# Optimization experiments

Hardware: AMD Instinct MI355X
Metric: run time of the kernel (lower is better)

## Reference

```python
import jax, jax.numpy as jnp
import numpy as np

NUM_USERS = 100000
NUM_ITEMS = 50000
NUM_NODES = NUM_USERS + NUM_ITEMS
EMBED_DIM = 64
NUM_LAYERS = 3
NUM_EDGES = 1200000


def setup_inputs() -> dict:
    key = jax.random.key(0)
    k1, k2 = jax.random.split(key)
    edge_index = jax.random.randint(k1, (2, NUM_EDGES), 0, NUM_NODES, dtype=jnp.int32)
    # xavier_uniform for [N, D]
    limit = float(np.sqrt(6.0 / (NUM_NODES + EMBED_DIM)))
    embedding = jax.random.uniform(k2, (NUM_NODES, EMBED_DIM), dtype=jnp.float32,
                                   minval=-limit, maxval=limit)
    return {"edge_index": edge_index, "embedding": embedding}


def reference(edge_index, embedding):
    n = embedding.shape[0]
    row, col = edge_index[0], edge_index[1]
    ones = jnp.ones((edge_index.shape[1],), dtype=embedding.dtype)
    deg_row = jax.ops.segment_sum(ones, row, num_segments=n)
    deg_col = jax.ops.segment_sum(ones, col, num_segments=n)
    # deg^-0.5 with inf (deg==0) -> 0
    inv_row = jnp.where(deg_row > 0, jax.lax.rsqrt(jnp.maximum(deg_row, 1e-30)), 0.0)
    inv_col = jnp.where(deg_col > 0, jax.lax.rsqrt(jnp.maximum(deg_col, 1e-30)), 0.0)
    norm = (inv_row[row] * inv_col[col])[:, None]  # [E, 1]

    x = embedding
    accum = x
    for _ in range(NUM_LAYERS):
        # gather source embeddings, scale by symmetric norm, scatter-add at target
        msgs = norm * x[row]                       # [E, D]
        x = jax.ops.segment_sum(msgs, col, num_segments=n)
        accum = accum + x
    final = accum / jnp.asarray(NUM_LAYERS + 1, dtype=embedding.dtype)
    return final[:NUM_USERS], final[NUM_USERS:]
```

## Files before the change

kernel.cpp:

```cpp
#include <hip/hip_runtime.h>
#include <hip/hip_fp16.h>


constexpr int NUM_USERS = 100000;
constexpr int NUM_ITEMS = 50000;
constexpr int N_NODES   = NUM_USERS + NUM_ITEMS;
constexpr int EMBED_DIM = 64;
constexpr int NUM_EDGES = 1200000;
constexpr int SHIFT = 9;
constexpr int BSZ   = 1 << SHIFT;
constexpr int NBUCK = (N_NODES + BSZ - 1) >> SHIFT;
constexpr int EPB   = 8192;
constexpr int P1_BLOCKS = (NUM_EDGES + EPB - 1) / EPB;
constexpr int CAPB  = 64;
constexpr int FIXCAP  = 32;
constexpr int FIXHALF = 16;

__global__ void __launch_bounds__(1024)
pass1_bin(const int4* __restrict__ row4, const int4* __restrict__ col4,
          unsigned int* __restrict__ binned_c, unsigned short* __restrict__ binned_r,
          int* __restrict__ cnts_c, int* __restrict__ cnts_r) {
    __shared__ int cur_c[NBUCK], cur_r[NBUCK];
    int t = threadIdx.x, blk = blockIdx.x;
    for (int i = t; i < NBUCK; i += 1024) { cur_c[i] = 0; cur_r[i] = 0; }
    __syncthreads();
    constexpr int NV = NUM_EDGES / 4;
    int base4 = blk * 2048;
#pragma unroll
    for (int k = 0; k < 2; ++k) {
        int v = base4 + k * 1024 + t;
        if (v < NV) {
            int4 c = col4[v];
            int4 r = row4[v];
            int cc[4] = {c.x, c.y, c.z, c.w};
            int rr[4] = {r.x, r.y, r.z, r.w};
#pragma unroll
            for (int q = 0; q < 4; ++q) {
                int dc = cc[q] >> SHIFT;
                int sc = atomicAdd(&cur_c[dc], 1);
                if (sc < CAPB)
                    binned_c[(dc * P1_BLOCKS + blk) * CAPB + sc] =
                        ((unsigned)(cc[q] & (BSZ - 1)) << 18) | (unsigned)rr[q];
                int dr = rr[q] >> SHIFT;
                int sr = atomicAdd(&cur_r[dr], 1);
                if (sr < CAPB)
                    binned_r[(dr * P1_BLOCKS + blk) * CAPB + sr] =
                        (unsigned short)(rr[q] & (BSZ - 1));
            }
        }
    }
    __syncthreads();
    for (int i = t; i < NBUCK; i += 1024) {
        cnts_c[blk * NBUCK + i] = cur_c[i];
        cnts_r[blk * NBUCK + i] = cur_r[i];
    }
}

__global__ void __launch_bounds__(512)
pass2_place(const unsigned int* __restrict__ binned_c, const unsigned short* __restrict__ binned_r,
            const int* __restrict__ cnts_c, const int* __restrict__ cnts_r,
            int* __restrict__ fixed_idx, ushort2* __restrict__ deg2) {
    __shared__ int cur[BSZ];
    __shared__ int cnt_l[P1_BLOCKS];
    int t = threadIdx.x;
    cur[t] = 0;
    int b = blockIdx.x;
    constexpr int TOT = P1_BLOCKS * CAPB;
    if (b < NBUCK) {
        for (int i = t; i < P1_BLOCKS; i += 512) cnt_l[i] = cnts_c[i * NBUCK + b];
        __syncthreads();
        const unsigned int* src = binned_c + (size_t)b * TOT;
        for (int i = t; i < TOT; i += 512) {
            int cnt = cnt_l[i >> 6]; if (cnt > CAPB) cnt = CAPB;
            if ((i & 63) < cnt) {
                unsigned int w = src[i];
                int lc = (int)(w >> 18);
                int r  = (int)(w & 0x3FFFFu);
                int slot = atomicAdd(&cur[lc], 1);
                if (slot < FIXCAP)
                    fixed_idx[(((b << SHIFT) | lc) << 5) + slot] = r;
            }
        }
        __syncthreads();
        int node = (b << SHIFT) + t;
        if (node < N_NODES) deg2[node].x = (unsigned short)cur[t];
    } else {
        int bb = b - NBUCK;
        for (int i = t; i < P1_BLOCKS; i += 512) cnt_l[i] = cnts_r[i * NBUCK + bb];
        __syncthreads();
        const unsigned short* src = binned_r + (size_t)bb * TOT;
        for (int i = t; i < TOT; i += 512) {
            int cnt = cnt_l[i >> 6]; if (cnt > CAPB) cnt = CAPB;
            if ((i & 63) < cnt) atomicAdd(&cur[src[i]], 1);
        }
        __syncthreads();
        int node = (bb << SHIFT) + t;
        if (node < N_NODES) deg2[node].y = (unsigned short)cur[t];
    }
}

__global__ void init_y_kernel(const unsigned int* __restrict__ deg2w,
                              const float4* __restrict__ emb4, int2* __restrict__ y0) {
    int i = blockIdx.x * blockDim.x + threadIdx.x;
    if (i < N_NODES * (EMBED_DIM / 4)) {
        int dr = (int)(deg2w[i >> 4] >> 16);
        float w = (dr > 0) ? rsqrtf((float)dr) : 0.0f;
        float4 e = emb4[i];
        __half2 h0 = __floats2half2_rn(w * e.x, w * e.y);
        __half2 h1 = __floats2half2_rn(w * e.z, w * e.w);
        y0[i] = make_int2(*reinterpret_cast<int*>(&h0), *reinterpret_cast<int*>(&h1));
    }
}

__device__ __forceinline__ void acc8(float* f, const int4& v) {
    float2 a0 = __half22float2(*reinterpret_cast<const __half2*>(&v.x));
    float2 a1 = __half22float2(*reinterpret_cast<const __half2*>(&v.y));
    float2 a2 = __half22float2(*reinterpret_cast<const __half2*>(&v.z));
    float2 a3 = __half22float2(*reinterpret_cast<const __half2*>(&v.w));
    f[0] += a0.x; f[1] += a0.y; f[2] += a1.x; f[3] += a1.y;
    f[4] += a2.x; f[5] += a2.y; f[6] += a3.x; f[7] += a3.y;
}

__global__ void __launch_bounds__(256, 8)
layer_kernel(const unsigned int* __restrict__ deg2w,
             const int* __restrict__ fixed_idx,
             const int4* __restrict__ y_src,
             int4* __restrict__ y_dst,
             int4* __restrict__ x_acc,
             float4* __restrict__ out4,
             const float4* __restrict__ emb4,
             int mode) {
    int wv = (blockIdx.x * blockDim.x + threadIdx.x) >> 6;
    int nA = wv << 1;
    if (nA >= N_NODES) return;
    int nB = nA | 1;
    int lane = threadIdx.x & 63;
    int d4 = lane & 7;
    int e  = lane >> 3;
    int sl = lane & 15;

    int recA = fixed_idx[(nA << 5) | sl];
    int recB = fixed_idx[(nB << 5) | sl];
    uint2 dd = reinterpret_cast<const uint2*>(deg2w)[wv];
    int4 xv;
    float4 o0, o1;
    if (e == 2 || e == 3) {
        int n = (e == 2) ? nA : nB;
        if (mode != 0) xv = x_acc[n * 8 + d4];
        if (mode == 2) { o0 = emb4[n * 16 + d4 * 2]; o1 = emb4[n * 16 + d4 * 2 + 1]; }
    }

    int crA = (int)(dd.x & 0xFFFFu), drA = (int)(dd.x >> 16);
    int crB = (int)(dd.y & 0xFFFFu), drB = (int)(dd.y >> 16);
    int cntA = (crA < FIXCAP) ? crA : FIXCAP;
    int cntB = (crB < FIXCAP) ? crB : FIXCAP;
    float invcA = (crA > 0) ? rsqrtf((float)crA) : 0.0f;
    float invcB = (crB > 0) ? rsqrtf((float)crB) : 0.0f;
    float invrA = (drA > 0) ? rsqrtf((float)drA) : 0.0f;
    float invrB = (drB > 0) ? rsqrtf((float)drB) : 0.0f;
    int idxA = (sl < cntA) ? recA : 0;
    int idxB = (sl < cntB) ? recB : 0;

    float fA[8] = {0.f, 0.f, 0.f, 0.f, 0.f, 0.f, 0.f, 0.f};
    float fB[8] = {0.f, 0.f, 0.f, 0.f, 0.f, 0.f, 0.f, 0.f};

    if (cntA <= FIXHALF && cntB <= FIXHALF) {
        int s0A = __shfl(idxA, e);
        int s1A = __shfl(idxA, 8 + e);
        int s0B = __shfl(idxB, e);
        int s1B = __shfl(idxB, 8 + e);
        int4 vaA = y_src[s0A * 8 + d4];
        int4 vbA = y_src[s1A * 8 + d4];
        int4 vaB = y_src[s0B * 8 + d4];
        int4 vbB = y_src[s1B * 8 + d4];
        if (e < cntA)     acc8(fA, vaA);
        if (8 + e < cntA) acc8(fA, vbA);
        if (e < cntB)     acc8(fB, vaB);
        if (8 + e < cntB) acc8(fB, vbB);
    } else {
        {
            int rec2 = fixed_idx[(nA << 5) | 16 | sl];
            int idx2 = ((16 | sl) < cntA) ? rec2 : 0;
            int s0 = __shfl(idxA, e),     s1 = __shfl(idxA, 8 + e);
            int s2 = __shfl(idx2, e),     s3 = __shfl(idx2, 8 + e);
            int4 va = y_src[s0 * 8 + d4], vb = y_src[s1 * 8 + d4];
            int4 vc = y_src[s2 * 8 + d4], vd = y_src[s3 * 8 + d4];
            if (e < cntA)      acc8(fA, va);
            if (8 + e < cntA)  acc8(fA, vb);
            if (16 + e < cntA) acc8(fA, vc);
            if (24 + e < cntA) acc8(fA, vd);
        }
        {
            int rec2 = fixed_idx[(nB << 5) | 16 | sl];
            int idx2 = ((16 | sl) < cntB) ? rec2 : 0;
            int s0 = __shfl(idxB, e),     s1 = __shfl(idxB, 8 + e);
            int s2 = __shfl(idx2, e),     s3 = __shfl(idx2, 8 + e);
            int4 va = y_src[s0 * 8 + d4], vb = y_src[s1 * 8 + d4];
            int4 vc = y_src[s2 * 8 + d4], vd = y_src[s3 * 8 + d4];
            if (e < cntB)      acc8(fB, va);
            if (8 + e < cntB)  acc8(fB, vb);
            if (16 + e < cntB) acc8(fB, vc);
            if (24 + e < cntB) acc8(fB, vd);
        }
    }

#pragma unroll
    for (int k = 0; k < 8; ++k) {
        fA[k] += __shfl_xor(fA[k], 8);
        fA[k] += __shfl_xor(fA[k], 16);
        fA[k] += __shfl_xor(fA[k], 32);
        fB[k] += __shfl_xor(fB[k], 8);
        fB[k] += __shfl_xor(fB[k], 16);
        fB[k] += __shfl_xor(fB[k], 32);
    }
#pragma unroll
    for (int k = 0; k < 8; ++k) { fA[k] *= invcA; fB[k] *= invcB; }

    if (mode != 2) {
        if (e == 0 || e == 1) {
            int n = (e == 0) ? nA : nB;
            float invr = (e == 0) ? invrA : invrB;
            const float* f = (e == 0) ? fA : fB;
            __half2 p0 = __floats2half2_rn(invr * f[0], invr * f[1]);
            __half2 p1 = __floats2half2_rn(invr * f[2], invr * f[3]);
            __half2 p2 = __floats2half2_rn(invr * f[4], invr * f[5]);
            __half2 p3 = __floats2half2_rn(invr * f[6], invr * f[7]);
            int4 st;
            st.x = *reinterpret_cast<int*>(&p0);
            st.y = *reinterpret_cast<int*>(&p1);
            st.z = *reinterpret_cast<int*>(&p2);
            st.w = *reinterpret_cast<int*>(&p3);
            y_dst[n * 8 + d4] = st;
        } else if (e == 2 || e == 3) {
            int n = (e == 2) ? nA : nB;
            const float* f = (e == 2) ? fA : fB;
            float g[8];
            if (mode == 1) {
                float2 b0 = __half22float2(*reinterpret_cast<const __half2*>(&xv.x));
                float2 b1 = __half22float2(*reinterpret_cast<const __half2*>(&xv.y));
                float2 b2 = __half22float2(*reinterpret_cast<const __half2*>(&xv.z));
                float2 b3 = __half22float2(*reinterpret_cast<const __half2*>(&xv.w));
                g[0] = b0.x + f[0]; g[1] = b0.y + f[1]; g[2] = b1.x + f[2]; g[3] = b1.y + f[3];
                g[4] = b2.x + f[4]; g[5] = b2.y + f[5]; g[6] = b3.x + f[6]; g[7] = b3.y + f[7];
            } else {
#pragma unroll
                for (int k = 0; k < 8; ++k) g[k] = f[k];
            }
            __half2 q0 = __floats2half2_rn(g[0], g[1]);
            __half2 q1 = __floats2half2_rn(g[2], g[3]);
            __half2 q2 = __floats2half2_rn(g[4], g[5]);
            __half2 q3 = __floats2half2_rn(g[6], g[7]);
            int4 st;
            st.x = *reinterpret_cast<int*>(&q0);
            st.y = *reinterpret_cast<int*>(&q1);
            st.z = *reinterpret_cast<int*>(&q2);
            st.w = *reinterpret_cast<int*>(&q3);
            x_acc[n * 8 + d4] = st;
        }
    } else if (e == 2 || e == 3) {
        int n = (e == 2) ? nA : nB;
        const float* f = (e == 2) ? fA : fB;
        float2 b0 = __half22float2(*reinterpret_cast<const __half2*>(&xv.x));
        float2 b1 = __half22float2(*reinterpret_cast<const __half2*>(&xv.y));
        float2 b2 = __half22float2(*reinterpret_cast<const __half2*>(&xv.z));
        float2 b3 = __half22float2(*reinterpret_cast<const __half2*>(&xv.w));
        o0.x = (o0.x + b0.x + f[0]) * 0.25f; o0.y = (o0.y + b0.y + f[1]) * 0.25f;
        o0.z = (o0.z + b1.x + f[2]) * 0.25f; o0.w = (o0.w + b1.y + f[3]) * 0.25f;
        o1.x = (o1.x + b2.x + f[4]) * 0.25f; o1.y = (o1.y + b2.y + f[5]) * 0.25f;
        o1.z = (o1.z + b3.x + f[6]) * 0.25f; o1.w = (o1.w + b3.y + f[7]) * 0.25f;
        int ob = n * 16 + d4 * 2;
        out4[ob]     = o0;
        out4[ob + 1] = o1;
    }
}

extern "C" void kernel_launch(void* const* d_in, const int* in_sizes, int n_in,
                              void* d_out, int out_size, void* d_ws, size_t ws_size,
                              hipStream_t stream) {
    const int*   edge_index = (const int*)d_in[0];
    const float* embedding  = (const float*)d_in[1];
    const int* row = edge_index;
    const int* col = edge_index + NUM_EDGES;
    float* out = (float*)d_out;

    char* ws = (char*)d_ws;
    auto align_up = [](size_t v) { return (v + 255) & ~size_t(255); };
    size_t off = 0;
    ushort2* deg2    = (ushort2*)(ws + off); off = align_up(off + sizeof(ushort2) * N_NODES);
    int* cnts_c      = (int*)(ws + off); off = align_up(off + sizeof(int) * P1_BLOCKS * NBUCK);
    int* cnts_r      = (int*)(ws + off); off = align_up(off + sizeof(int) * P1_BLOCKS * NBUCK);
    int* fixed_idx   = (int*)(ws + off); off = align_up(off + sizeof(int) * N_NODES * FIXCAP);
    __half2* ya      = (__half2*)(ws + off); off = align_up(off + sizeof(__half2) * N_NODES * 32);
    __half2* yb      = (__half2*)(ws + off); off = align_up(off + sizeof(__half2) * N_NODES * 32);
    __half2* xa      = (__half2*)(ws + off); off = align_up(off + sizeof(__half2) * N_NODES * 32);
    unsigned int*   binned_c = (unsigned int*)d_out;
    unsigned short* binned_r = (unsigned short*)ya;

    pass1_bin<<<P1_BLOCKS, 1024, 0, stream>>>((const int4*)row, (const int4*)col,
                                              binned_c, binned_r, cnts_c, cnts_r);
    pass2_place<<<2 * NBUCK, 512, 0, stream>>>(binned_c, binned_r, cnts_c, cnts_r,
                                               fixed_idx, deg2);
    {
        int n4 = N_NODES * 16;
        int threads = 256, blocks = (n4 + threads - 1) / threads;
        init_y_kernel<<<blocks, threads, 0, stream>>>((const unsigned int*)deg2,
                                                      (const float4*)embedding, (int2*)ya);
    }
    {
        int threads = 256;
        int blocks = (N_NODES / 2 * 64 + threads - 1) / threads;
        layer_kernel<<<blocks, threads, 0, stream>>>((const unsigned int*)deg2, fixed_idx,
                                                     (const int4*)ya, (int4*)yb, (int4*)xa,
                                                     (float4*)out, (const float4*)embedding, 0);
        layer_kernel<<<blocks, threads, 0, stream>>>((const unsigned int*)deg2, fixed_idx,
                                                     (const int4*)yb, (int4*)ya, (int4*)xa,
                                                     (float4*)out, (const float4*)embedding, 1);
        layer_kernel<<<blocks, threads, 0, stream>>>((const unsigned int*)deg2, fixed_idx,
                                                     (const int4*)ya, (int4*)yb , (int4*)xa,
                                                     (float4*)out, (const float4*)embedding, 2);
    }
}
```

Measured before the change: 254.9 us.

## Fuse init scaling into pass2 and shrink binning blocks

The separate init_y kernel is folded into the row-degree half of pass2_place, which scales the embeddings by the in-shared-memory degree right after counting, removing one launch and the global deg2 read. Pass1 now bins 2048 edges per block with 256 threads and a per-bucket capacity of 32, giving more blocks and smaller binned buffers. The row-bin scratch moves from ya to xa so ya can be written during pass2. A smaller capacity raises the chance of per-block bucket overflow, and the cap clamp on the count was removed.

```diff
diff --git a/kernel.cpp b/kernel.cpp
--- a/kernel.cpp
+++ b/kernel.cpp
@@ -10,25 +10,25 @@
 constexpr int SHIFT = 9;
 constexpr int BSZ   = 1 << SHIFT;
 constexpr int NBUCK = (N_NODES + BSZ - 1) >> SHIFT;
-constexpr int EPB   = 8192;
+constexpr int EPB   = 2048;
 constexpr int P1_BLOCKS = (NUM_EDGES + EPB - 1) / EPB;
-constexpr int CAPB  = 64;
+constexpr int CAPB  = 32;
 constexpr int FIXCAP  = 32;
 constexpr int FIXHALF = 16;
 
-__global__ void __launch_bounds__(1024)
+__global__ void __launch_bounds__(256)
 pass1_bin(const int4* __restrict__ row4, const int4* __restrict__ col4,
           unsigned int* __restrict__ binned_c, unsigned short* __restrict__ binned_r,
           int* __restrict__ cnts_c, int* __restrict__ cnts_r) {
     __shared__ int cur_c[NBUCK], cur_r[NBUCK];
     int t = threadIdx.x, blk = blockIdx.x;
-    for (int i = t; i < NBUCK; i += 1024) { cur_c[i] = 0; cur_r[i] = 0; }
+    for (int i = t; i < NBUCK; i += 256) { cur_c[i] = 0; cur_r[i] = 0; }
     __syncthreads();
     constexpr int NV = NUM_EDGES / 4;
-    int base4 = blk * 2048;
+    int base4 = blk * (EPB / 4);
 #pragma unroll
     for (int k = 0; k < 2; ++k) {
-        int v = base4 + k * 1024 + t;
+        int v = base4 + k * 256 + t;
         if (v < NV) {
             int4 c = col4[v];
             int4 r = row4[v];
@@ -50,7 +50,7 @@
         }
     }
     __syncthreads();
-    for (int i = t; i < NBUCK; i += 1024) {
+    for (int i = t; i < NBUCK; i += 256) {
         cnts_c[blk * NBUCK + i] = cur_c[i];
         cnts_r[blk * NBUCK + i] = cur_r[i];
     }
@@ -59,7 +59,8 @@
 __global__ void __launch_bounds__(512)
 pass2_place(const unsigned int* __restrict__ binned_c, const unsigned short* __restrict__ binned_r,
             const int* __restrict__ cnts_c, const int* __restrict__ cnts_r,
-            int* __restrict__ fixed_idx, ushort2* __restrict__ deg2) {
+            int* __restrict__ fixed_idx, ushort2* __restrict__ deg2,
+            const float4* __restrict__ emb4, int4* __restrict__ y0) {
     __shared__ int cur[BSZ];
     __shared__ int cnt_l[P1_BLOCKS];
     int t = threadIdx.x;
@@ -71,8 +72,8 @@
         __syncthreads();
         const unsigned int* src = binned_c + (size_t)b * TOT;
         for (int i = t; i < TOT; i += 512) {
-            int cnt = cnt_l[i >> 6]; if (cnt > CAPB) cnt = CAPB;
-            if ((i & 63) < cnt) {
+            int cnt = cnt_l[i >> 5];
+            if ((i & 31) < cnt) {
                 unsigned int w = src[i];
                 int lc = (int)(w >> 18);
                 int r  = (int)(w & 0x3FFFFu);
@@ -90,25 +91,32 @@
         __syncthreads();
         const unsigned short* src = binned_r + (size_t)bb * TOT;
         for (int i = t; i < TOT; i += 512) {
-            int cnt = cnt_l[i >> 6]; if (cnt > CAPB) cnt = CAPB;
-            if ((i & 63) < cnt) atomicAdd(&cur[src[i]], 1);
+            int cnt = cnt_l[i >> 5];
+            if ((i & 31) < cnt) atomicAdd(&cur[src[i]], 1);
         }
         __syncthreads();
         int node = (bb << SHIFT) + t;
         if (node < N_NODES) deg2[node].y = (unsigned short)cur[t];
-    }
-}
-
-__global__ void init_y_kernel(const unsigned int* __restrict__ deg2w,
-                              const float4* __restrict__ emb4, int2* __restrict__ y0) {
-    int i = blockIdx.x * blockDim.x + threadIdx.x;
-    if (i < N_NODES * (EMBED_DIM / 4)) {
-        int dr = (int)(deg2w[i >> 4] >> 16);
-        float w = (dr > 0) ? rsqrtf((float)dr) : 0.0f;
-        float4 e = emb4[i];
-        __half2 h0 = __floats2half2_rn(w * e.x, w * e.y);
-        __half2 h1 = __floats2half2_rn(w * e.z, w * e.w);
-        y0[i] = make_int2(*reinterpret_cast<int*>(&h0), *reinterpret_cast<int*>(&h1));
+        for (int i = t; i < BSZ * 8; i += 512) {
+            int n = (bb << SHIFT) + (i >> 3);
+            if (n < N_NODES) {
+                int dr = cur[i >> 3];
+                float w = (dr > 0) ? rsqrtf((float)dr) : 0.0f;
+                int p = (i & 7) * 2;
+                float4 e0 = emb4[n * 16 + p];
+                float4 e1 = emb4[n * 16 + p + 1];
+                __half2 h0 = __floats2half2_rn(w * e0.x, w * e0.y);
+                __half2 h1 = __floats2half2_rn(w * e0.z, w * e0.w);
+                __half2 h2 = __floats2half2_rn(w * e1.x, w * e1.y);
+                __half2 h3 = __floats2half2_rn(w * e1.z, w * e1.w);
+                int4 st;
+                st.x = *reinterpret_cast<int*>(&h0);
+                st.y = *reinterpret_cast<int*>(&h1);
+                st.z = *reinterpret_cast<int*>(&h2);
+                st.w = *reinterpret_cast<int*>(&h3);
+                y0[n * 8 + (i & 7)] = st;
+            }
+        }
     }
 }
 
@@ -294,18 +302,13 @@
     __half2* yb      = (__half2*)(ws + off); off = align_up(off + sizeof(__half2) * N_NODES * 32);
     __half2* xa      = (__half2*)(ws + off); off = align_up(off + sizeof(__half2) * N_NODES * 32);
     unsigned int*   binned_c = (unsigned int*)d_out;
-    unsigned short* binned_r = (unsigned short*)ya;
-
-    pass1_bin<<<P1_BLOCKS, 1024, 0, stream>>>((const int4*)row, (const int4*)col,
-                                              binned_c, binned_r, cnts_c, cnts_r);
+    unsigned short* binned_r = (unsigned short*)xa;
+
+    pass1_bin<<<P1_BLOCKS, 256, 0, stream>>>((const int4*)row, (const int4*)col,
+                                             binned_c, binned_r, cnts_c, cnts_r);
     pass2_place<<<2 * NBUCK, 512, 0, stream>>>(binned_c, binned_r, cnts_c, cnts_r,
-                                               fixed_idx, deg2);
-    {
-        int n4 = N_NODES * 16;
-        int threads = 256, blocks = (n4 + threads - 1) / threads;
-        init_y_kernel<<<blocks, threads, 0, stream>>>((const unsigned int*)deg2,
-                                                      (const float4*)embedding, (int2*)ya);
-    }
+                                               fixed_idx, deg2,
+                                               (const float4*)embedding, (int4*)ya);
     {
         int threads = 256;
         int blocks = (N_NODES / 2 * 64 + threads - 1) / threads;
```

Result: slower. 273.7 us (+7.4%).
